# Performance work log

Hardware: AMD Instinct MI355X
Metric: run time of the kernel (lower is better)

The kernel has to match this reference:

```python
import jax, jax.numpy as jnp
import numpy as np
import math

B, S, D, H = 32, 4096, 512, 8
HD = D // H          # head_dim = 64
NUM_NODES = 15       # (1 << tree_depth) - 1
SPARSITY = 0.7


def _pruned(rng, out_f, in_f):
    w = (rng.standard_normal((out_f, in_f)) / np.sqrt(in_f)).astype(np.float32)
    thr = np.quantile(np.abs(w), SPARSITY)
    return jnp.asarray(np.where(np.abs(w) >= thr, w, 0.0))


def _posenc(seq_len, d):
    pos = np.arange(seq_len)[:, None].astype(np.float32)
    div = np.exp(np.arange(0, d, 2).astype(np.float32) * (-math.log(10000.0) / d))
    pe = np.zeros((seq_len, d), np.float32)
    pe[:, 0::2] = np.sin(pos * div)
    pe[:, 1::2] = np.cos(pos * div)
    return jnp.asarray(pe[None])  # [1, S, D]


def setup_inputs() -> dict:
    rng = np.random.default_rng(0)
    key = jax.random.key(0)
    f = lambda shape: jnp.asarray((rng.standard_normal(shape) * 0.02).astype(np.float32))
    node_w = jnp.stack([_pruned(rng, HD, HD) for _ in range(NUM_NODES)])  # [15, hd, hd]
    return dict(
        text_input=jax.random.randint(key, (B, S), 0, 256),
        pe=_posenc(S, D),
        id_w=f((D,)), id_b=f((D,)),                 # Linear(1, D) weight/bias
        eg=jnp.ones((D,)), ebeta=jnp.zeros((D,)),   # embed_norm
        sub_w=_pruned(rng, D, D), sub_b=f((D,)),
        sub_th=jnp.ones((D,)), sub_tau=jnp.full((D,), 0.5), sub_vr=jnp.zeros((D,)),
        sub_ng=jnp.ones((D,)), sub_nb=jnp.zeros((D,)),
        word_w=_pruned(rng, D, D), word_b=f((D,)),
        word_th=jnp.ones((D,)), word_tau=jnp.full((D,), 0.5), word_vr=jnp.zeros((D,)),
        word_ng=jnp.ones((D,)), word_nb=jnp.zeros((D,)),
        qkv_w=_pruned(rng, 3 * D, D), qkv_b=f((3 * D,)),
        node_w=node_w, node_b=f((NUM_NODES, HD)),
        node_th=jnp.ones((NUM_NODES, HD)), node_tau=jnp.full((NUM_NODES, HD), 0.5),
        node_vr=jnp.zeros((NUM_NODES, HD)),
        out_ng=jnp.ones((D,)), out_nb=jnp.zeros((D,)),
    )


def _ln(x, g, b, eps=1e-5):
    m = x.mean(-1, keepdims=True)
    v = ((x - m) ** 2).mean(-1, keepdims=True)
    return (x - m) / jnp.sqrt(v + eps) * g + b


def _fuse(x, w, b, th, ng, nb, gs):
    # mean-pool groups of gs, sparse linear, LIF gate (zero initial membrane -> v = x), residual + LN
    bb, L, d = x.shape
    fused = x.reshape(bb, L // gs, gs, d).mean(2)
    proj = fused @ w.T + b
    spike = (proj >= th).astype(x.dtype)  # eval-mode LIF spike
    return _ln(proj * spike + fused, ng, nb)


def _tree(seq, nw, nb, th, tau, vr, states):
    # seq: [B, H, L, hd]; binary tree of depth 4: 16 leaf chunks, only first 8 map to nodes 7..14
    bb, hh, L, hd = seq.shape
    leaves = seq.reshape(bb, hh, 16, L // 16, hd)[:, :, :8]  # [B, H, 8, sub, hd]
    ranges = ((7, 15), (3, 7), (1, 3), (0, 1))  # node index ranges per level (leaf -> root)
    out = None
    new_states = []
    for lvl, (lo, hi) in enumerate(ranges):
        inp = leaves if lvl == 0 else 0.5 * (out[:, :, 0::2] + out[:, :, 1::2])
        proj = jnp.einsum('bhnsd,ned->bhnse', inp, nw[lo:hi]) + nb[lo:hi][None, None, :, None, :]
        v = tau[lo:hi][None, None, :, None, :] * states[lvl] + proj  # LIF membrane update
        sp = (v >= th[lo:hi][None, None, :, None, :]).astype(seq.dtype)
        new_states.append(v * (1.0 - sp) + vr[lo:hi][None, None, :, None, :] * sp)
        out = proj * sp
    return out[:, :, 0], new_states  # root: [B, H, sub, hd]


def reference(text_input, pe, id_w, id_b, eg, ebeta, sub_w, sub_b, sub_th, sub_tau, sub_vr,
              sub_ng, sub_nb, word_w, word_b, word_th, word_tau, word_vr, word_ng, word_nb,
              qkv_w, qkv_b, node_w, node_b, node_th, node_tau, node_vr, out_ng, out_nb):
    bb, ss = text_input.shape
    d = id_w.shape[0]
    hd = node_w.shape[-1]
    h = d // hd
    ids = text_input.astype(jnp.float32)[..., None]            # [B, S, 1]
    x = _ln(ids * id_w + id_b + pe[:, :ss], eg, ebeta)         # char embeddings [B, S, D]
    sub = _fuse(x, sub_w, sub_b, sub_th, sub_ng, sub_nb, 2)    # [B, S/2, D]
    word = _fuse(sub, word_w, word_b, word_th, word_ng, word_nb, 4)  # [B, S/8, D]
    L = word.shape[1]  # 512, power of two -> no q/k/v padding needed
    qkv = (word @ qkv_w.T + qkv_b).reshape(bb, L, 3, h, hd).transpose(2, 0, 3, 1, 4)
    q, k, v = qkv[0], qkv[1], qkv[2]                            # [B, H, L, hd]
    zstates = [jnp.zeros((bb, h, n, L // 16, hd), x.dtype) for n in (8, 4, 2, 1)]
    tree_k, st = _tree(k, node_w, node_b, node_th, node_tau, node_vr, zstates)
    tree_v, _ = _tree(v, node_w, node_b, node_th, node_tau, node_vr, st)  # membrane state carried from K pass
    scores = jnp.einsum('bhqd,bhkd->bhqk', q, tree_k) / math.sqrt(hd)     # [B, H, L, sub]
    attn = jnp.einsum('bhqk,bhkd->bhqd', jax.nn.softmax(scores, -1), tree_v)
    out = _ln(attn.transpose(0, 2, 1, 3).reshape(bb, L, d) + word, out_ng, out_nb)
    # F.interpolate(mode='linear', align_corners=False): L -> S along sequence axis
    src = jnp.maximum((jnp.arange(S) + 0.5) * (L / S) - 0.5, 0.0)
    i0 = jnp.floor(src).astype(jnp.int32)
    i1 = jnp.minimum(i0 + 1, L - 1)
    w1 = (src - i0.astype(src.dtype))[None, :, None]
    return out[:, i0] * (1.0 - w1) + out[:, i1] * w1  # [B, S, D]
```

## Files before the change

kernel.cpp:

```cpp
#include <hip/hip_runtime.h>
#include <math.h>


__device__ __forceinline__ float fadd32(float a, float b) { return __fadd_rn(a, b); }
__device__ __forceinline__ float fmul32(float a, float b) { return __fmul_rn(a, b); }
__device__ __forceinline__ float fsub32(float a, float b) { return __fsub_rn(a, b); }
__device__ __forceinline__ float fdiv32(float a, float b) { return __fdiv_rn(a, b); }

__device__ __forceinline__ void gload16(const float* g, float* l) {
  __builtin_amdgcn_global_load_lds(
      (const __attribute__((address_space(1))) void*)g,
      (__attribute__((address_space(3))) void*)l, 16, 0, 0);
}

__device__ __forceinline__ float np_pairwise512(const float* row, int lane) {
  const int L = lane >> 4, j = lane & 15;
  const float* p = row + 128 * L + j;
  const float r0 = p[0],  r1 = p[16], r2 = p[32],  r3 = p[48];
  const float r4 = p[64], r5 = p[80], r6 = p[96],  r7 = p[112];
  float v = fadd32(fadd32(fadd32(r0, r1), fadd32(r2, r3)),
                   fadd32(fadd32(r4, r5), fadd32(r6, r7)));
  v = fadd32(v, __shfl_xor(v, 8));
  v = fadd32(v, __shfl_xor(v, 4));
  v = fadd32(v, __shfl_xor(v, 2));
  v = fadd32(v, __shfl_xor(v, 1));
  v = fadd32(v, __shfl_xor(v, 16));
  v = fadd32(v, __shfl_xor(v, 32));
  return v;
}

__global__ __launch_bounds__(256) void k_embed(
    const int* __restrict__ text, const float* __restrict__ pe,
    const float* __restrict__ id_w, const float* __restrict__ id_b,
    const float* __restrict__ eg, const float* __restrict__ eb,
    float* __restrict__ fused) {
  __shared__ float rb[4][512];
  const int w = threadIdx.x >> 6;
  const int lane = threadIdx.x & 63;
  const int wid = blockIdx.x * 4 + w;
  const int b = wid >> 11;
  const int t = wid & 2047;
  const int c0 = lane * 4, c1 = 256 + lane * 4;
  const float4 iw0 = *(const float4*)&id_w[c0], iw1 = *(const float4*)&id_w[c1];
  const float4 ib0 = *(const float4*)&id_b[c0], ib1 = *(const float4*)&id_b[c1];
  const float4 g0  = *(const float4*)&eg[c0],  g1  = *(const float4*)&eg[c1];
  const float4 e0  = *(const float4*)&eb[c0],  e1  = *(const float4*)&eb[c1];
  float4 fus0, fus1;
#pragma unroll
  for (int ss = 0; ss < 2; ++ss) {
    const int s = 2 * t + ss;
    const float idv = (float)text[b * 4096 + s];
    const float4 p0 = *(const float4*)&pe[(size_t)s * 512 + c0];
    const float4 p1 = *(const float4*)&pe[(size_t)s * 512 + c1];
    float4 x0, x1;
#pragma unroll
    for (int j = 0; j < 4; ++j) {
      (&x0.x)[j] = fadd32(fadd32(fmul32(idv, (&iw0.x)[j]), (&ib0.x)[j]), (&p0.x)[j]);
      (&x1.x)[j] = fadd32(fadd32(fmul32(idv, (&iw1.x)[j]), (&ib1.x)[j]), (&p1.x)[j]);
    }
    *(float4*)&rb[w][c0] = x0;
    *(float4*)&rb[w][c1] = x1;
    const float m = fmul32(np_pairwise512(rb[w], lane), 1.f / 512.f);
    float4 d0, d1, q0, q1;
#pragma unroll
    for (int j = 0; j < 4; ++j) {
      (&d0.x)[j] = fsub32((&x0.x)[j], m);
      (&d1.x)[j] = fsub32((&x1.x)[j], m);
      (&q0.x)[j] = fmul32((&d0.x)[j], (&d0.x)[j]);
      (&q1.x)[j] = fmul32((&d1.x)[j], (&d1.x)[j]);
    }
    *(float4*)&rb[w][c0] = q0;
    *(float4*)&rb[w][c1] = q1;
    const float var = fmul32(np_pairwise512(rb[w], lane), 1.f / 512.f);
    const float sdev = __fsqrt_rn(fadd32(var, 1e-5f));
#pragma unroll
    for (int j = 0; j < 4; ++j) {
      const float l0 = fadd32(fmul32(fdiv32((&d0.x)[j], sdev), (&g0.x)[j]), (&e0.x)[j]);
      const float l1 = fadd32(fmul32(fdiv32((&d1.x)[j], sdev), (&g1.x)[j]), (&e1.x)[j]);
      if (ss) {
        (&fus0.x)[j] = fmul32(fadd32((&fus0.x)[j], l0), 0.5f);
        (&fus1.x)[j] = fmul32(fadd32((&fus1.x)[j], l1), 0.5f);
      } else {
        (&fus0.x)[j] = l0;
        (&fus1.x)[j] = l1;
      }
    }
  }
  const size_t row = (size_t)wid * 512;
  *(float4*)&fused[row + c0] = fus0;
  *(float4*)&fused[row + c1] = fus1;
}

__global__ __launch_bounds__(256) void k_transpose_w(
    const float* __restrict__ W, float* __restrict__ WT, int Nn) {
  __shared__ float t[32][33];
  const int n0 = blockIdx.x * 32, k0 = blockIdx.y * 32;
  const int li = threadIdx.x & 31, wi = threadIdx.x >> 5;
  for (int r = wi; r < 32; r += 8)
    t[r][li] = W[(size_t)(n0 + r) * 512 + k0 + li];
  __syncthreads();
  for (int r = wi; r < 32; r += 8)
    WT[(size_t)(k0 + r) * Nn + n0 + li] = t[li][r];
}

#define GEMM_INNER(acc, buf)                                         \
  _Pragma("unroll")                                                  \
  for (int kq = 0; kq < 32; kq += 4) {                               \
    float4 xf[4];                                                    \
    _Pragma("unroll")                                                \
    for (int r = 0; r < 4; ++r)                                      \
      xf[r] = *(const float4*)&Xs[buf][rg * 4 + r][kq];              \
    _Pragma("unroll")                                                \
    for (int u = 0; u < 4; ++u) {                                    \
      const float4 w0 = *(const float4*)&Ws[buf][kq + u][cg * 4];    \
      const float4 w1 = *(const float4*)&Ws[buf][kq + u][128 + cg * 4]; \
      _Pragma("unroll")                                              \
      for (int r = 0; r < 4; ++r) {                                  \
        const float xv = (&xf[r].x)[u];                              \
        acc[r][0] = __fmaf_rn(xv, w0.x, acc[r][0]);                  \
        acc[r][1] = __fmaf_rn(xv, w0.y, acc[r][1]);                  \
        acc[r][2] = __fmaf_rn(xv, w0.z, acc[r][2]);                  \
        acc[r][3] = __fmaf_rn(xv, w0.w, acc[r][3]);                  \
        acc[r][4] = __fmaf_rn(xv, w1.x, acc[r][4]);                  \
        acc[r][5] = __fmaf_rn(xv, w1.y, acc[r][5]);                  \
        acc[r][6] = __fmaf_rn(xv, w1.z, acc[r][6]);                  \
        acc[r][7] = __fmaf_rn(xv, w1.w, acc[r][7]);                  \
      }                                                              \
    }                                                                \
  }

#define STAGE(buf, k0)                                                        \
  {                                                                           \
    gload16(&X[(bm + wvid * 8 + (lane >> 3)) * 512 + (k0) + (lane & 7) * 4],  \
            &Xs[buf][wvid * 8][0]);                                           \
    _Pragma("unroll")                                                         \
    for (int c = 0; c < 4; ++c)                                               \
      gload16(&WT[(size_t)((k0) + wvid * 4 + c) * N + bn + lane * 4],         \
              &Ws[buf][wvid * 4 + c][0]);                                     \
  }

__global__ __launch_bounds__(512) void k_gemm_nt(
    const float* __restrict__ X, const float* __restrict__ WT,
    const float* __restrict__ bias, const float* __restrict__ th,
    float* __restrict__ OUT, int N) {
  __shared__ float Xs[2][64][32];
  __shared__ float Ws[2][32][256];
  const int tid = threadIdx.x;
  const int wvid = tid >> 6, lane = tid & 63;
  const int rg = tid >> 5;
  const int cg = tid & 31;
  const size_t bm = (size_t)blockIdx.x * 64;
  const int bn = blockIdx.y * 256;

  float accA[4][8], accB[4][8];
#pragma unroll
  for (int r = 0; r < 4; ++r)
#pragma unroll
    for (int c = 0; c < 8; ++c) { accA[r][c] = 0.f; accB[r][c] = 0.f; }

  STAGE(0, 0);
  asm volatile("s_waitcnt vmcnt(0)" ::: "memory");
  asm volatile("s_barrier" ::: "memory");
  for (int t = 0; t < 16; ++t) {
    const int cur = t & 1;
    if (t < 15) {
      STAGE(cur ^ 1, (t + 1) * 32);
      asm volatile("s_waitcnt vmcnt(5)" ::: "memory");
    } else {
      asm volatile("s_waitcnt vmcnt(0)" ::: "memory");
    }
    asm volatile("s_barrier" ::: "memory");
    if (t < 12) { GEMM_INNER(accA, cur); } else { GEMM_INNER(accB, cur); }
    asm volatile("s_barrier" ::: "memory");
  }
#pragma unroll
  for (int r = 0; r < 4; ++r) {
    const size_t rb = (bm + rg * 4 + r) * (size_t)N;
    float4 o0, o1;
#pragma unroll
    for (int c = 0; c < 4; ++c) {
      const int col0 = bn + cg * 4 + c;
      const int col1 = bn + 128 + cg * 4 + c;
      const float v0 = fadd32(fadd32(accA[r][c], accB[r][c]), bias[col0]);
      const float v1 = fadd32(fadd32(accA[r][4 + c], accB[r][4 + c]), bias[col1]);
      (&o0.x)[c] = th ? ((v0 >= th[col0]) ? v0 : 0.f) : v0;
      (&o1.x)[c] = th ? ((v1 >= th[col1]) ? v1 : 0.f) : v1;
    }
    *(float4*)&OUT[rb + bn + cg * 4] = o0;
    *(float4*)&OUT[rb + bn + 128 + cg * 4] = o1;
  }
}

__global__ __launch_bounds__(256) void k_add_ln(
    const float* __restrict__ A, const float* F,
    const float* __restrict__ g, const float* __restrict__ bet,
    float* O, int nrows) {
  __shared__ float zb[4][512];
  const int w = threadIdx.x >> 6;
  const int lane = threadIdx.x & 63;
  const int wid = blockIdx.x * 4 + w;
  if (wid >= nrows) return;
  const size_t row = (size_t)wid * 512;
  const int c0 = lane * 4, c1 = 256 + lane * 4;
  const float4 a0 = *(const float4*)&A[row + c0];
  const float4 a1 = *(const float4*)&A[row + c1];
  const float4 f0 = *(const float4*)&F[row + c0];
  const float4 f1 = *(const float4*)&F[row + c1];
  float4 z0, z1;
#pragma unroll
  for (int j = 0; j < 4; ++j) {
    (&z0.x)[j] = fadd32((&a0.x)[j], (&f0.x)[j]);
    (&z1.x)[j] = fadd32((&a1.x)[j], (&f1.x)[j]);
  }
  *(float4*)&zb[w][c0] = z0;
  *(float4*)&zb[w][c1] = z1;
  const float m = fmul32(np_pairwise512(zb[w], lane), 1.f / 512.f);
  float4 d0, d1, q0, q1;
#pragma unroll
  for (int j = 0; j < 4; ++j) {
    (&d0.x)[j] = fsub32((&z0.x)[j], m);
    (&d1.x)[j] = fsub32((&z1.x)[j], m);
    (&q0.x)[j] = fmul32((&d0.x)[j], (&d0.x)[j]);
    (&q1.x)[j] = fmul32((&d1.x)[j], (&d1.x)[j]);
  }
  *(float4*)&zb[w][c0] = q0;
  *(float4*)&zb[w][c1] = q1;
  const float var = fmul32(np_pairwise512(zb[w], lane), 1.f / 512.f);
  const float sdev = __fsqrt_rn(fadd32(var, 1e-5f));
  const float4 gg0 = *(const float4*)&g[c0], gg1 = *(const float4*)&g[c1];
  const float4 bb0 = *(const float4*)&bet[c0], bb1 = *(const float4*)&bet[c1];
  float4 o0, o1;
#pragma unroll
  for (int j = 0; j < 4; ++j) {
    (&o0.x)[j] = fadd32(fmul32(fdiv32((&d0.x)[j], sdev), (&gg0.x)[j]), (&bb0.x)[j]);
    (&o1.x)[j] = fadd32(fmul32(fdiv32((&d1.x)[j], sdev), (&gg1.x)[j]), (&bb1.x)[j]);
  }
  *(float4*)&O[row + c0] = o0;
  *(float4*)&O[row + c1] = o1;
}

__global__ __launch_bounds__(256) void k_add_ln_pool(
    const float* __restrict__ A, const float* __restrict__ F,
    const float* __restrict__ g, const float* __restrict__ bet,
    float* __restrict__ OUT) {
  __shared__ float zb[4][512];
  __shared__ float lnr[4][512];
  const int w = threadIdx.x >> 6;
  const int lane = threadIdx.x & 63;
  const int wid = blockIdx.x * 4 + w;
  const size_t row = (size_t)wid * 512;
  const int c0 = lane * 4, c1 = 256 + lane * 4;
  const float4 a0 = *(const float4*)&A[row + c0];
  const float4 a1 = *(const float4*)&A[row + c1];
  const float4 f0 = *(const float4*)&F[row + c0];
  const float4 f1 = *(const float4*)&F[row + c1];
  float4 z0, z1;
#pragma unroll
  for (int j = 0; j < 4; ++j) {
    (&z0.x)[j] = fadd32((&a0.x)[j], (&f0.x)[j]);
    (&z1.x)[j] = fadd32((&a1.x)[j], (&f1.x)[j]);
  }
  *(float4*)&zb[w][c0] = z0;
  *(float4*)&zb[w][c1] = z1;
  const float m = fmul32(np_pairwise512(zb[w], lane), 1.f / 512.f);
  float4 d0, d1, q0, q1;
#pragma unroll
  for (int j = 0; j < 4; ++j) {
    (&d0.x)[j] = fsub32((&z0.x)[j], m);
    (&d1.x)[j] = fsub32((&z1.x)[j], m);
    (&q0.x)[j] = fmul32((&d0.x)[j], (&d0.x)[j]);
    (&q1.x)[j] = fmul32((&d1.x)[j], (&d1.x)[j]);
  }
  *(float4*)&zb[w][c0] = q0;
  *(float4*)&zb[w][c1] = q1;
  const float var = fmul32(np_pairwise512(zb[w], lane), 1.f / 512.f);
  const float sdev = __fsqrt_rn(fadd32(var, 1e-5f));
  float4 o0, o1;
#pragma unroll
  for (int j = 0; j < 4; ++j) {
    (&o0.x)[j] = fadd32(fmul32(fdiv32((&d0.x)[j], sdev), g[c0 + j]), bet[c0 + j]);
    (&o1.x)[j] = fadd32(fmul32(fdiv32((&d1.x)[j], sdev), g[c1 + j]), bet[c1 + j]);
  }
  *(float4*)&lnr[w][c0] = o0;
  *(float4*)&lnr[w][c1] = o1;
  __syncthreads();
  if (threadIdx.x < 128) {
    const int c4 = threadIdx.x * 4;
    const float4 l0 = *(const float4*)&lnr[0][c4];
    const float4 l1 = *(const float4*)&lnr[1][c4];
    const float4 l2 = *(const float4*)&lnr[2][c4];
    const float4 l3 = *(const float4*)&lnr[3][c4];
    float4 o;
#pragma unroll
    for (int j = 0; j < 4; ++j) {
      const float s = fadd32(fadd32(fadd32((&l0.x)[j], (&l1.x)[j]), (&l2.x)[j]),
                             (&l3.x)[j]);
      (&o.x)[j] = fmul32(s, 0.25f);
    }
    *(float4*)&OUT[(size_t)blockIdx.x * 512 + c4] = o;
  }
}

__global__ __launch_bounds__(256) void k_transpose_nw(
    const float* __restrict__ nw, float* __restrict__ nwT) {
  const int idx = blockIdx.x * 256 + threadIdx.x;
  if (idx >= 15 * 4096) return;
  const int n = idx >> 12;
  const int e = (idx >> 6) & 63;
  const int d = idx & 63;
  nwT[(n << 12) + (d << 6) + e] = nw[idx];
}

#define NP_EINSUM64(inp, wp, out_)                                          \
  {                                                                         \
    float c0 = 0.f, c1 = 0.f, c2 = 0.f, c3 = 0.f;                           \
    _Pragma("unroll")                                                       \
    for (int q_ = 0; q_ < 4; ++q_) {                                        \
      const int b_ = 16 * q_;                                               \
      _Pragma("unroll")                                                     \
      for (int u_ = 3; u_ >= 0; --u_) {                                     \
        const int d0_ = b_ + 4 * u_;                                        \
        c0 = fadd32(fmul32(__shfl(inp, d0_ + 0), wp[(d0_ + 0) << 6]), c0);  \
        c1 = fadd32(fmul32(__shfl(inp, d0_ + 1), wp[(d0_ + 1) << 6]), c1);  \
        c2 = fadd32(fmul32(__shfl(inp, d0_ + 2), wp[(d0_ + 2) << 6]), c2);  \
        c3 = fadd32(fmul32(__shfl(inp, d0_ + 3), wp[(d0_ + 3) << 6]), c3);  \
      }                                                                     \
    }                                                                       \
    out_ = fadd32(fadd32(c0, c1), fadd32(c2, c3));                          \
  }

__global__ __launch_bounds__(256) void k_tree(
    const float* __restrict__ QKV, const float* __restrict__ nwT,
    const float* __restrict__ nb, const float* __restrict__ th,
    const float* __restrict__ tau, const float* __restrict__ vr,
    float* __restrict__ TK, float* __restrict__ TV) {
  __shared__ float st0[8][8][64];
  __shared__ float st1[4][8][64];
  __shared__ float st2[2][8][64];
  __shared__ float st3[8][64];
  __shared__ float outA[8][8][64];
  __shared__ float outB[4][8][64];
  const int tid = threadIdx.x, w = tid >> 6, lane = tid & 63;
  const int sq = blockIdx.x & 3, bh = blockIdx.x >> 2;
  const int b = bh >> 3, h = bh & 7;
  for (int pass = 0; pass < 2; ++pass) {
    const int koff = 512 + pass * 512;
    for (int r = w; r < 64; r += 4) {
      const int n = r >> 3, sl = r & 7, sg = sq * 8 + sl;
      const float inp = QKV[((size_t)(b * 512 + n * 32 + sg)) * 1536 + koff + h * 64 + lane];
      const int node = 7 + n, pc = node * 64 + lane;
      const float* wp = nwT + node * 4096 + lane;
      float tot;
      NP_EINSUM64(inp, wp, tot);
      const float proj = fadd32(tot, nb[pc]);
      const float v = pass ? fadd32(fmul32(tau[pc], st0[n][sl][lane]), proj) : proj;
      const bool sp = v >= th[pc];
      if (!pass) st0[n][sl][lane] = sp ? vr[pc] : v;
      outA[n][sl][lane] = sp ? proj : 0.f;
    }
    __syncthreads();
    for (int r = w; r < 32; r += 4) {
      const int n = r >> 3, sl = r & 7;
      const float inp = fmul32(0.5f, fadd32(outA[2 * n][sl][lane], outA[2 * n + 1][sl][lane]));
      const int node = 3 + n, pc = node * 64 + lane;
      const float* wp = nwT + node * 4096 + lane;
      float tot;
      NP_EINSUM64(inp, wp, tot);
      const float proj = fadd32(tot, nb[pc]);
      const float v = pass ? fadd32(fmul32(tau[pc], st1[n][sl][lane]), proj) : proj;
      const bool sp = v >= th[pc];
      if (!pass) st1[n][sl][lane] = sp ? vr[pc] : v;
      outB[n][sl][lane] = sp ? proj : 0.f;
    }
    __syncthreads();
    for (int r = w; r < 16; r += 4) {
      const int n = r >> 3, sl = r & 7;
      const float inp = fmul32(0.5f, fadd32(outB[2 * n][sl][lane], outB[2 * n + 1][sl][lane]));
      const int node = 1 + n, pc = node * 64 + lane;
      const float* wp = nwT + node * 4096 + lane;
      float tot;
      NP_EINSUM64(inp, wp, tot);
      const float proj = fadd32(tot, nb[pc]);
      const float v = pass ? fadd32(fmul32(tau[pc], st2[n][sl][lane]), proj) : proj;
      const bool sp = v >= th[pc];
      if (!pass) st2[n][sl][lane] = sp ? vr[pc] : v;
      outA[n][sl][lane] = sp ? proj : 0.f;
    }
    __syncthreads();
    for (int r = w; r < 8; r += 4) {
      const int sl = r & 7, sg = sq * 8 + sl;
      const float inp = fmul32(0.5f, fadd32(outA[0][sl][lane], outA[1][sl][lane]));
      const int pc = lane;
      const float* wp = nwT + lane;
      float tot;
      NP_EINSUM64(inp, wp, tot);
      const float proj = fadd32(tot, nb[pc]);
      const float v = pass ? fadd32(fmul32(tau[pc], st3[sl][lane]), proj) : proj;
      const bool sp = v >= th[pc];
      if (!pass) st3[sl][lane] = sp ? vr[pc] : v;
      float* dst = pass ? TV : TK;
      dst[((size_t)bh * 32 + sg) * 64 + lane] = sp ? proj : 0.f;
    }
    __syncthreads();
  }
}

__global__ __launch_bounds__(256) void k_attn(
    const float* __restrict__ qkv, const float* __restrict__ treeK,
    const float* __restrict__ treeV, float* __restrict__ attn) {
  __shared__ float Ks[32][65];
  __shared__ float Vs[32][64];
  __shared__ float qs[4][64];
  const int tid = threadIdx.x;
  const int bh = blockIdx.x >> 7;
  const int lq0 = (blockIdx.x & 127) * 4;
  const int b = bh >> 3, h = bh & 7;
  for (int i = tid; i < 2048; i += 256) {
    const int j = i >> 6, d = i & 63;
    Ks[j][d] = treeK[((size_t)bh * 32 + j) * 64 + d];
    Vs[j][d] = treeV[((size_t)bh * 32 + j) * 64 + d];
  }
  {
    const int w = tid >> 6, d = tid & 63;
    qs[w][d] = qkv[((size_t)(b * 512) + lq0 + w) * 1536 + h * 64 + d];
  }
  __syncthreads();
  const int w = tid >> 6;
  const int lane = tid & 63;
  const int j = lane & 31;
  float sc = 0.f;
#pragma unroll
  for (int d = 0; d < 64; ++d) sc = __fmaf_rn(qs[w][d], Ks[j][d], sc);
  sc = fmul32(sc, 0.125f);
  float m = sc;
#pragma unroll
  for (int k = 1; k < 32; k <<= 1) m = fmaxf(m, __shfl_xor(m, k));
  float p = expf(fsub32(sc, m));
  float sum = p;
#pragma unroll
  for (int k = 1; k < 32; k <<= 1) sum += __shfl_xor(sum, k);
  p = fdiv32(p, sum);
  float acc = 0.f;
#pragma unroll
  for (int jj = 0; jj < 32; ++jj)
    acc = __fmaf_rn(__shfl(p, jj), Vs[jj][lane], acc);
  attn[((size_t)(b * 512) + lq0 + w) * 512 + h * 64 + lane] = acc;
}

__global__ __launch_bounds__(256) void k_interp(
    const float* __restrict__ rows, float* __restrict__ out) {
  const int wid = blockIdx.x * 4 + (threadIdx.x >> 6);
  const int lane = threadIdx.x & 63;
  const int b = wid >> 12;
  const int s = wid & 4095;
  const double src = fmax(((double)s + 0.5) * 0.125 - 0.5, 0.0);
  const int i0 = (int)src;
  const int i1 = min(i0 + 1, 511);
  const double w1 = src - (double)i0;
  const double w0 = 1.0 - w1;
  const size_t r0 = ((size_t)b * 512 + i0) * 512;
  const size_t r1 = ((size_t)b * 512 + i1) * 512;
  const size_t o = (size_t)wid * 512;
#pragma unroll
  for (int k = 0; k < 2; ++k) {
    const int c4 = lane + 64 * k;
    const float4 a = *reinterpret_cast<const float4*>(&rows[r0 + (size_t)c4 * 4]);
    const float4 c = *reinterpret_cast<const float4*>(&rows[r1 + (size_t)c4 * 4]);
    float4 r;
    r.x = (float)((double)a.x * w0 + (double)c.x * w1);
    r.y = (float)((double)a.y * w0 + (double)c.y * w1);
    r.z = (float)((double)a.z * w0 + (double)c.z * w1);
    r.w = (float)((double)a.w * w0 + (double)c.w * w1);
    *reinterpret_cast<float4*>(&out[o + (size_t)c4 * 4]) = r;
  }
}

extern "C" void kernel_launch(void* const* d_in, const int* in_sizes, int n_in,
                              void* d_out, int out_size, void* d_ws, size_t ws_size,
                              hipStream_t stream) {
  const int*   text    = (const int*)d_in[0];
  const float* pe      = (const float*)d_in[1];
  const float* id_w    = (const float*)d_in[2];
  const float* id_b    = (const float*)d_in[3];
  const float* eg      = (const float*)d_in[4];
  const float* ebeta   = (const float*)d_in[5];
  const float* sub_w   = (const float*)d_in[6];
  const float* sub_b   = (const float*)d_in[7];
  const float* sub_th  = (const float*)d_in[8];
  const float* sub_ng  = (const float*)d_in[11];
  const float* sub_nb  = (const float*)d_in[12];
  const float* word_w  = (const float*)d_in[13];
  const float* word_b  = (const float*)d_in[14];
  const float* word_th = (const float*)d_in[15];
  const float* word_ng = (const float*)d_in[18];
  const float* word_nb = (const float*)d_in[19];
  const float* qkv_w   = (const float*)d_in[20];
  const float* qkv_b   = (const float*)d_in[21];
  const float* node_w  = (const float*)d_in[22];
  const float* node_b  = (const float*)d_in[23];
  const float* node_th = (const float*)d_in[24];
  const float* node_tau= (const float*)d_in[25];
  const float* node_vr = (const float*)d_in[26];
  const float* out_ng  = (const float*)d_in[27];
  const float* out_nb  = (const float*)d_in[28];

  float* O   = (float*)d_out;
  float* WSF = (float*)d_ws;

  float* FU  = O;
  float* GZ1 = O + 33554432;
  float* WD  = O + 33554432;
  float* GZ2 = O + 41943040;
  float* QKV = O + 41943040;

  float* W1   = WSF;
  float* NWT  = WSF + 8388608;
  float* TK   = WSF + 8450048;
  float* TV   = WSF + 8974336;
  float* ROWS = WSF + 9498624;
  float* WTs  = WSF + 17887232;
  float* WTw  = WSF + 18149376;
  float* WTq  = WSF + 18411520;
  float* ATT  = WSF;

  k_transpose_w<<<dim3(16, 16), 256, 0, stream>>>(sub_w, WTs, 512);
  k_transpose_w<<<dim3(16, 16), 256, 0, stream>>>(word_w, WTw, 512);
  k_transpose_w<<<dim3(48, 16), 256, 0, stream>>>(qkv_w, WTq, 1536);
  k_transpose_nw<<<240, 256, 0, stream>>>(node_w, NWT);
  k_embed<<<16384, 256, 0, stream>>>(text, pe, id_w, id_b, eg, ebeta, FU);
  k_gemm_nt<<<dim3(1024, 2), 512, 0, stream>>>(FU, WTs, sub_b, sub_th, GZ1, 512);
  k_add_ln_pool<<<16384, 256, 0, stream>>>(GZ1, FU, sub_ng, sub_nb, W1);
  k_gemm_nt<<<dim3(256, 2), 512, 0, stream>>>(W1, WTw, word_b, word_th, GZ2, 512);
  k_add_ln<<<4096, 256, 0, stream>>>(GZ2, W1, word_ng, word_nb, WD, 16384);
  k_gemm_nt<<<dim3(256, 6), 512, 0, stream>>>(WD, WTq, qkv_b, nullptr, QKV, 1536);
  k_tree<<<1024, 256, 0, stream>>>(QKV, NWT, node_b, node_th,
                                   node_tau, node_vr, TK, TV);
  k_attn<<<32768, 256, 0, stream>>>(QKV, TK, TV, ATT);
  k_add_ln<<<4096, 256, 0, stream>>>(ATT, WD, out_ng, out_nb, ROWS, 16384);
  k_interp<<<32768, 256, 0, stream>>>(ROWS, O);
}
```

Baseline: 1.868 ms.

## Read GEMM X operand via wave-uniform scalar loads instead of LDS staging

New measurement: 2.519 ms. 34.9% more time.

```diff
diff --git a/kernel.cpp b/kernel.cpp
--- a/kernel.cpp
+++ b/kernel.cpp
@@ -103,60 +103,51 @@
     WT[(size_t)(k0 + r) * Nn + n0 + li] = t[li][r];
 }
 
-#define GEMM_INNER(acc, buf)                                         \
+#define GEMM_INNER(acc, buf, k0g)                                    \
   _Pragma("unroll")                                                  \
   for (int kq = 0; kq < 32; kq += 4) {                               \
-    float4 xf[4];                                                    \
+    float4 wq[4];                                                    \
     _Pragma("unroll")                                                \
-    for (int r = 0; r < 4; ++r)                                      \
-      xf[r] = *(const float4*)&Xs[buf][rg * 4 + r][kq];              \
+    for (int u = 0; u < 4; ++u)                                      \
+      wq[u] = *(const float4*)&Ws[buf][kq + u][lane * 4];            \
     _Pragma("unroll")                                                \
     for (int u = 0; u < 4; ++u) {                                    \
-      const float4 w0 = *(const float4*)&Ws[buf][kq + u][cg * 4];    \
-      const float4 w1 = *(const float4*)&Ws[buf][kq + u][128 + cg * 4]; \
       _Pragma("unroll")                                              \
-      for (int r = 0; r < 4; ++r) {                                  \
-        const float xv = (&xf[r].x)[u];                              \
-        acc[r][0] = __fmaf_rn(xv, w0.x, acc[r][0]);                  \
-        acc[r][1] = __fmaf_rn(xv, w0.y, acc[r][1]);                  \
-        acc[r][2] = __fmaf_rn(xv, w0.z, acc[r][2]);                  \
-        acc[r][3] = __fmaf_rn(xv, w0.w, acc[r][3]);                  \
-        acc[r][4] = __fmaf_rn(xv, w1.x, acc[r][4]);                  \
-        acc[r][5] = __fmaf_rn(xv, w1.y, acc[r][5]);                  \
-        acc[r][6] = __fmaf_rn(xv, w1.z, acc[r][6]);                  \
-        acc[r][7] = __fmaf_rn(xv, w1.w, acc[r][7]);                  \
+      for (int r = 0; r < 8; ++r) {                                  \
+        const float xv = xbase[r * 512 + (k0g) + kq + u];            \
+        acc[r][0] = __fmaf_rn(xv, wq[u].x, acc[r][0]);               \
+        acc[r][1] = __fmaf_rn(xv, wq[u].y, acc[r][1]);               \
+        acc[r][2] = __fmaf_rn(xv, wq[u].z, acc[r][2]);               \
+        acc[r][3] = __fmaf_rn(xv, wq[u].w, acc[r][3]);               \
       }                                                              \
     }                                                                \
   }
 
 #define STAGE(buf, k0)                                                        \
   {                                                                           \
-    gload16(&X[(bm + wvid * 8 + (lane >> 3)) * 512 + (k0) + (lane & 7) * 4],  \
-            &Xs[buf][wvid * 8][0]);                                           \
     _Pragma("unroll")                                                         \
     for (int c = 0; c < 4; ++c)                                               \
-      gload16(&WT[(size_t)((k0) + wvid * 4 + c) * N + bn + lane * 4],         \
-              &Ws[buf][wvid * 4 + c][0]);                                     \
+      gload16(&WT[(size_t)((k0) + wvu * 4 + c) * N + bn + lane * 4],          \
+              &Ws[buf][wvu * 4 + c][0]);                                      \
   }
 
 __global__ __launch_bounds__(512) void k_gemm_nt(
     const float* __restrict__ X, const float* __restrict__ WT,
     const float* __restrict__ bias, const float* __restrict__ th,
     float* __restrict__ OUT, int N) {
-  __shared__ float Xs[2][64][32];
   __shared__ float Ws[2][32][256];
   const int tid = threadIdx.x;
-  const int wvid = tid >> 6, lane = tid & 63;
-  const int rg = tid >> 5;
-  const int cg = tid & 31;
+  const int lane = tid & 63;
+  const int wvu = __builtin_amdgcn_readfirstlane(tid >> 6);
   const size_t bm = (size_t)blockIdx.x * 64;
   const int bn = blockIdx.y * 256;
-
-  float accA[4][8], accB[4][8];
-#pragma unroll
-  for (int r = 0; r < 4; ++r)
-#pragma unroll
-    for (int c = 0; c < 8; ++c) { accA[r][c] = 0.f; accB[r][c] = 0.f; }
+  const float* __restrict__ xbase = X + (bm + (size_t)wvu * 8) * 512;
+
+  float accA[8][4], accB[8][4];
+#pragma unroll
+  for (int r = 0; r < 8; ++r)
+#pragma unroll
+    for (int c = 0; c < 4; ++c) { accA[r][c] = 0.f; accB[r][c] = 0.f; }
 
   STAGE(0, 0);
   asm volatile("s_waitcnt vmcnt(0)" ::: "memory");
@@ -165,29 +156,27 @@
     const int cur = t & 1;
     if (t < 15) {
       STAGE(cur ^ 1, (t + 1) * 32);
-      asm volatile("s_waitcnt vmcnt(5)" ::: "memory");
+      asm volatile("s_waitcnt vmcnt(4)" ::: "memory");
     } else {
       asm volatile("s_waitcnt vmcnt(0)" ::: "memory");
     }
     asm volatile("s_barrier" ::: "memory");
-    if (t < 12) { GEMM_INNER(accA, cur); } else { GEMM_INNER(accB, cur); }
+    if (t < 12) { GEMM_INNER(accA, cur, t * 32); }
+    else        { GEMM_INNER(accB, cur, t * 32); }
     asm volatile("s_barrier" ::: "memory");
   }
 #pragma unroll
-  for (int r = 0; r < 4; ++r) {
-    const size_t rb = (bm + rg * 4 + r) * (size_t)N;
-    float4 o0, o1;
+  for (int r = 0; r < 8; ++r) {
+    const size_t orow = (bm + wvu * 8 + r) * (size_t)N + bn + lane * 4;
+    float4 o;
+    float* op = &o.x;
 #pragma unroll
     for (int c = 0; c < 4; ++c) {
-      const int col0 = bn + cg * 4 + c;
-      const int col1 = bn + 128 + cg * 4 + c;
-      const float v0 = fadd32(fadd32(accA[r][c], accB[r][c]), bias[col0]);
-      const float v1 = fadd32(fadd32(accA[r][4 + c], accB[r][4 + c]), bias[col1]);
-      (&o0.x)[c] = th ? ((v0 >= th[col0]) ? v0 : 0.f) : v0;
-      (&o1.x)[c] = th ? ((v1 >= th[col1]) ? v1 : 0.f) : v1;
-    }
-    *(float4*)&OUT[rb + bn + cg * 4] = o0;
-    *(float4*)&OUT[rb + bn + 128 + cg * 4] = o1;
+      const int col = bn + lane * 4 + c;
+      const float v = fadd32(fadd32(accA[r][c], accB[r][c]), bias[col]);
+      op[c] = th ? ((v >= th[col]) ? v : 0.f) : v;
+    }
+    *(float4*)&OUT[orow] = o;
   }
 }
 
```
